# Kernel tuning notes

Measured on AMD Instinct MI355X. Metric: run time of the kernel, lower is better.

## Reference

```python
import math
import jax, jax.numpy as jnp
import numpy as np

B, N, L, D = 4, 16, 1024, 64  # batch, heads, seq len (L1=L2), head dim


def rel_shift(x):
    """Transformer-XL positional shift: [b,n,q,p]->[b,n,q,k] aligning relative positions."""
    b, n, q, k = x.shape
    x = jnp.pad(x, ((0, 0), (0, 0), (0, 0), (1, 0)))  # pad one zero column in front
    x = x.reshape(b, n, k + 1, q)
    return x[:, :, 1:, :].reshape(b, n, q, k)


def setup_inputs() -> dict:
    rng = jax.random.key(0)
    k1, k2, k3, k4, k5 = jax.random.split(rng, 5)
    query_content_biased = jax.random.normal(k1, (B, N, L, D), dtype=jnp.float32)
    query_pos_biased = jax.random.normal(k2, (B, N, L, D), dtype=jnp.float32)
    key = jax.random.normal(k3, (B, N, L, D), dtype=jnp.float32)
    value = jax.random.normal(k4, (B, N, L, D), dtype=jnp.float32)
    pos_encodings = jax.random.normal(k5, (N, L, D), dtype=jnp.float32)
    # causal mask: True = masked (as in torch masked_fill), broadcast over b,n
    mask = jnp.triu(jnp.ones((L, L), dtype=bool), k=1)[None, None]
    return {
        "query_content_biased": query_content_biased,
        "query_pos_biased": query_pos_biased,
        "key": key,
        "value": value,
        "pos_encodings": pos_encodings,
        "mask": mask,
    }


def reference(query_content_biased, query_pos_biased, key, value, pos_encodings, mask):
    # content scores: [b,n,i,j]
    weight = jnp.einsum('bnid,bnjd->bnij', query_content_biased, key)
    # positional scores, shifted into key axis
    pos_scores = jnp.einsum('bnid,npd->bnip', query_pos_biased, pos_encodings)
    weight = weight + rel_shift(pos_scores)
    weight = weight / math.sqrt(key.shape[-1])
    neg = jnp.finfo(weight.dtype).min
    weight = jnp.where(mask, neg, weight)
    weight = jax.nn.softmax(weight, axis=-1)
    weight = jnp.where(mask, jnp.zeros((), weight.dtype), weight)
    # dropout is identity at p=0.0 (eval)
    out = jnp.einsum('bnij,bnjd->bnid', weight, value)
    return (out, weight)
```

## Files before the change

kernel.cpp:

```cpp
#include <hip/hip_runtime.h>
#include <math.h>


#define Bq 4
#define Nh 16
#define Lq 1024
#define Dh 64
#define TQ 16
#define NT 512
#define LROW 1032

#define BAR() asm volatile("s_waitcnt lgkmcnt(0)\n\ts_barrier" ::: "memory")

typedef _Float16 h16;
typedef __attribute__((ext_vector_type(8))) _Float16 f16x8;
typedef __attribute__((ext_vector_type(4))) _Float16 f16x4;
typedef __attribute__((ext_vector_type(4))) float f32x4;

__device__ __forceinline__ f16x8 pack8h(float4 a, float4 b) {
    f16x8 o;
    o[0] = (h16)a.x; o[1] = (h16)a.y; o[2] = (h16)a.z; o[3] = (h16)a.w;
    o[4] = (h16)b.x; o[5] = (h16)b.y; o[6] = (h16)b.z; o[7] = (h16)b.w;
    return o;
}

__device__ __forceinline__ float wave_max(float v) {
    #pragma unroll
    for (int o = 32; o > 0; o >>= 1) v = fmaxf(v, __shfl_xor(v, o));
    return v;
}
__device__ __forceinline__ float wave_sum(float v) {
    #pragma unroll
    for (int o = 32; o > 0; o >>= 1) v += __shfl_xor(v, o);
    return v;
}

__global__ __launch_bounds__(256) void prep_kernel(
    const float* __restrict__ K, const float* __restrict__ P,
    const float* __restrict__ V,
    h16* __restrict__ Kb, h16* __restrict__ Pb, h16* __restrict__ Vt)
{
    __shared__ float t[64][65];
    int b = blockIdx.x;
    if (b < 5120) {
        const float* src; h16* dst; int idx;
        if (b < 4096) { idx = b * 256 + threadIdx.x; src = K; dst = Kb; }
        else          { idx = (b - 4096) * 256 + threadIdx.x; src = P; dst = Pb; }
        float4 v = ((const float4*)src)[idx];
        f16x4 o;
        o[0] = (h16)v.x; o[1] = (h16)v.y; o[2] = (h16)v.z; o[3] = (h16)v.w;
        ((f16x4*)dst)[idx] = o;
        return;
    }
    int bv = b - 5120;
    int bn = bv >> 4, jt = bv & 15;
    int tid = threadIdx.x;
    int d = tid & 63, q = tid >> 6;
    const float* vb = V + ((size_t)(bn * Lq + jt * 64)) * Dh;
    #pragma unroll
    for (int r = 0; r < 16; r++) {
        int jl = r * 4 + q;
        t[jl][d] = vb[(size_t)jl * Dh + d];
    }
    __syncthreads();
    int dd = tid >> 2, jb = (tid & 3) << 4;
    f16x8 s0, s1;
    #pragma unroll
    for (int jj = 0; jj < 8; jj++) {
        s0[jj] = (h16)t[jb + jj][dd];
        s1[jj] = (h16)t[jb + 8 + jj][dd];
    }
    h16* drow = Vt + (((size_t)(bn * 64 + dd)) << 10) + (jt << 6) + jb;
    *(f16x8*)drow = s0;
    *(f16x8*)(drow + 8) = s1;
}

__global__ __launch_bounds__(NT, 8) void relattn_kernel(
    const float* __restrict__ QC, const float* __restrict__ QP,
    const h16* __restrict__ Kb, const h16* __restrict__ Pb,
    const h16* __restrict__ Vtb,
    float* __restrict__ out, float* __restrict__ wout)
{
    __shared__ __align__(16) h16 s_s[TQ][LROW];
    __shared__ __align__(16) float dscr[4][64][4];

    const int tid  = threadIdx.x;
    const int w    = tid >> 6, lane = tid & 63;
    const int ln   = lane & 15, quad = lane >> 4;

    const int bidx = blockIdx.x;
    const int wg   = ((bidx & 7) << 9) | (bidx >> 3);
    const int bn   = wg >> 6, qt = 63 - (wg & 63);
    const int nh   = bn & 15;
    const int i0   = qt << 4, i1 = i0 + 15;

    const float* qcrow = QC + (((size_t)(bn << 10) + i0 + ln) << 6) + (quad << 3);
    const float* qprow = QP + (((size_t)(bn << 10) + i0 + ln) << 6) + (quad << 3);
    f16x8 aC0 = pack8h(*(const float4*)qcrow,        *(const float4*)(qcrow + 4));
    f16x8 aC1 = pack8h(*(const float4*)(qcrow + 32), *(const float4*)(qcrow + 36));
    f16x8 aP0 = pack8h(*(const float4*)qprow,        *(const float4*)(qprow + 4));
    f16x8 aP1 = pack8h(*(const float4*)(qprow + 32), *(const float4*)(qprow + 36));

    {
        f16x8 nf;
        #pragma unroll
        for (int k = 0; k < 8; k++) nf[k] = (h16)-INFINITY;
        int rr0 = tid >> 7;
        int tt  = tid & 127;
        int col = i0 + 16 + (tt << 3);
        if (col < 1024) {
            #pragma unroll
            for (int r = rr0; r < 16; r += 4)
                *(f16x8*)&s_s[r][col] = nf;
        }
    }

    const h16* kbase = Kb + (((size_t)(bn << 10)) << 6) + (quad << 3);
    #pragma unroll
    for (int ct = 0; ct < 8; ct++) {
        int c0 = ((ct << 3) + w) << 4;
        if (c0 <= i1) {
            const h16* kr = kbase + ((size_t)(c0 + ln) << 6);
            f32x4 acc = {0.f, 0.f, 0.f, 0.f};
            acc = __builtin_amdgcn_mfma_f32_16x16x32_f16(aC0, *(const f16x8*)kr,        acc, 0, 0, 0);
            acc = __builtin_amdgcn_mfma_f32_16x16x32_f16(aC1, *(const f16x8*)(kr + 32), acc, 0, 0, 0);
            #pragma unroll
            for (int rg = 0; rg < 4; rg++) {
                int row = (quad << 2) + rg;
                float val = (c0 + ln <= i0 + row) ? acc[rg] : -INFINITY;
                s_s[row][c0 + ln] = (h16)val;
            }
        }
    }
    BAR();

    const h16* pbase = Pb + (((size_t)(nh << 10)) << 6) + (quad << 3);
    #pragma unroll
    for (int ct = 0; ct < 8; ct++) {
        int p0 = ((ct << 3) + w) << 4;
        if (p0 + i0 + 30 >= 1023) {
            const h16* pr = pbase + ((size_t)(p0 + ln) << 6);
            f32x4 acc = {0.f, 0.f, 0.f, 0.f};
            acc = __builtin_amdgcn_mfma_f32_16x16x32_f16(aP0, *(const f16x8*)pr,        acc, 0, 0, 0);
            acc = __builtin_amdgcn_mfma_f32_16x16x32_f16(aP1, *(const f16x8*)(pr + 32), acc, 0, 0, 0);
            int p = p0 + ln;
            #pragma unroll
            for (int rg = 0; rg < 4; rg++) {
                int row = (quad << 2) + rg;
                int j = p + i0 + row - 1023;
                if (j >= 0)
                    s_s[row][j] = (h16)((float)s_s[row][j] + acc[rg]);
            }
        }
    }
    BAR();

    #pragma unroll
    for (int rr = 0; rr < 2; rr++) {
        int r = (w << 1) + rr;
        int i = i0 + r;
        float v[16];
        #pragma unroll
        for (int c = 0; c < 4; c++) {
            f16x4 t = *(f16x4*)&s_s[r][(c << 8) + (lane << 2)];
            v[c * 4 + 0] = (float)t[0]; v[c * 4 + 1] = (float)t[1];
            v[c * 4 + 2] = (float)t[2]; v[c * 4 + 3] = (float)t[3];
        }
        float mx = v[0];
        #pragma unroll
        for (int k = 1; k < 16; k++) mx = fmaxf(mx, v[k]);
        mx = wave_max(mx);
        float sum = 0.f;
        #pragma unroll
        for (int k = 0; k < 16; k++) {
            float t = __expf((v[k] - mx) * 0.125f);
            sum += t;
            v[k] = t;
        }
        sum = wave_sum(sum);
        float inv = __builtin_amdgcn_rcpf(sum);
        float* wrow = wout + (((size_t)(bn << 10) + i) << 10);
        #pragma unroll
        for (int c = 0; c < 4; c++) {
            int j = (c << 8) + (lane << 2);
            f32x4 e;
            e[0] = v[c * 4 + 0] * inv; e[1] = v[c * 4 + 1] * inv;
            e[2] = v[c * 4 + 2] * inv; e[3] = v[c * 4 + 3] * inv;
            __builtin_nontemporal_store(e, (f32x4*)&wrow[j]);
            f16x4 hh;
            hh[0] = (h16)e[0]; hh[1] = (h16)e[1]; hh[2] = (h16)e[2]; hh[3] = (h16)e[3];
            *(f16x4*)&s_s[r][j] = hh;
        }
    }
    BAR();

    f32x4 o = {0.f, 0.f, 0.f, 0.f};
    const int n0 = (w & 3) << 4;
    const int h  = w >> 2;
    const h16* vtb = Vtb + (((size_t)(bn << 6) + n0 + ln) << 10);
    const h16* abase = &s_s[ln][0];
    const int ksteps = (i0 + 16 + 31) >> 5;
    for (int ks = h; ks < ksteps; ks += 2) {
        int k0 = (ks << 5) + (quad << 3);
        f16x8 af = *(const f16x8*)(abase + k0);
        f16x8 vb = *(const f16x8*)(vtb + k0);
        o = __builtin_amdgcn_mfma_f32_16x16x32_f16(af, vb, o, 0, 0, 0);
    }
    if (h == 1)
        *(f32x4*)&dscr[w & 3][lane][0] = o;
    BAR();
    if (h == 0) {
        f32x4 o2 = *(f32x4*)&dscr[w][lane][0];
        o[0] += o2[0]; o[1] += o2[1]; o[2] += o2[2]; o[3] += o2[3];
        float* obase = out + (((size_t)(bn << 10) + i0) << 6);
        #pragma unroll
        for (int rg = 0; rg < 4; rg++)
            __builtin_nontemporal_store(
                o[rg], &obase[((size_t)((quad << 2) + rg) << 6) + n0 + ln]);
    }
}

extern "C" void kernel_launch(void* const* d_in, const int* in_sizes, int n_in,
                              void* d_out, int out_size, void* d_ws, size_t ws_size,
                              hipStream_t stream) {
    const float* qc = (const float*)d_in[0];
    const float* qp = (const float*)d_in[1];
    const float* K  = (const float*)d_in[2];
    const float* V  = (const float*)d_in[3];
    const float* P  = (const float*)d_in[4];

    float* out  = (float*)d_out;
    float* wout = out + (size_t)Bq * Nh * Lq * Dh;

    const size_t NQ = (size_t)Bq * Nh * Lq * Dh;
    const size_t NP = (size_t)Nh * Lq * Dh;
    h16* Kb  = (h16*)d_ws;
    h16* Pb  = Kb + NQ;
    h16* Vtb = Pb + NP;

    prep_kernel<<<4096 + 1024 + 1024, 256, 0, stream>>>(K, P, V, Kb, Pb, Vtb);
    relattn_kernel<<<Bq * Nh * (Lq / TQ), NT, 0, stream>>>(qc, qp, Kb, Pb, Vtb, out, wout);
}
```

Measured before the change: 432.5 us.

## Skip fully masked softmax chunks and zero masked weight tail in prep kernel

The attention kernel now handles only the 256-column chunks of each row up to the causal diagonal chunk, skipping -inf init, softmax and weight stores for fully masked chunks. The zero-filling of the masked upper region of the weight output moves into extra blocks of the prep kernel, which can overlap with the cast/transpose work. This cuts exp, LDS and store work in the main kernel. The same total bytes of weight output are still written, and the prep kernel grows by 4096 blocks.

```diff
diff --git a/kernel.cpp b/kernel.cpp
--- a/kernel.cpp
+++ b/kernel.cpp
@@ -38,23 +38,37 @@
 __global__ __launch_bounds__(256) void prep_kernel(
     const float* __restrict__ K, const float* __restrict__ P,
     const float* __restrict__ V,
-    h16* __restrict__ Kb, h16* __restrict__ Pb, h16* __restrict__ Vt)
+    h16* __restrict__ Kb, h16* __restrict__ Pb, h16* __restrict__ Vt,
+    float* __restrict__ wout)
 {
     __shared__ float t[64][65];
     int b = blockIdx.x;
+    int tid = threadIdx.x;
     if (b < 5120) {
         const float* src; h16* dst; int idx;
-        if (b < 4096) { idx = b * 256 + threadIdx.x; src = K; dst = Kb; }
-        else          { idx = (b - 4096) * 256 + threadIdx.x; src = P; dst = Pb; }
+        if (b < 4096) { idx = b * 256 + tid; src = K; dst = Kb; }
+        else          { idx = (b - 4096) * 256 + tid; src = P; dst = Pb; }
         float4 v = ((const float4*)src)[idx];
         f16x4 o;
         o[0] = (h16)v.x; o[1] = (h16)v.y; o[2] = (h16)v.z; o[3] = (h16)v.w;
         ((f16x4*)dst)[idx] = o;
         return;
     }
+    if (b >= 6144) {
+        int bv = b - 6144;
+        int bn = bv >> 6, qt = bv & 63;
+        int zstart = ((qt >> 4) + 1) << 8;
+        if (zstart >= 1024) return;
+        int row = tid >> 4;
+        int c0  = (tid & 15) << 2;
+        float* wr = wout + (((size_t)(bn << 10) + (qt << 4) + row) << 10);
+        f32x4 z = {0.f, 0.f, 0.f, 0.f};
+        for (int col = zstart + c0; col < 1024; col += 64)
+            __builtin_nontemporal_store(z, (f32x4*)&wr[col]);
+        return;
+    }
     int bv = b - 5120;
     int bn = bv >> 4, jt = bv & 15;
-    int tid = threadIdx.x;
     int d = tid & 63, q = tid >> 6;
     const float* vb = V + ((size_t)(bn * Lq + jt * 64)) * Dh;
     #pragma unroll
@@ -93,6 +107,8 @@
     const int bn   = wg >> 6, qt = 63 - (wg & 63);
     const int nh   = bn & 15;
     const int i0   = qt << 4, i1 = i0 + 15;
+    const int cmax = qt >> 4;
+    const int cend = (cmax + 1) << 8;
 
     const float* qcrow = QC + (((size_t)(bn << 10) + i0 + ln) << 6) + (quad << 3);
     const float* qprow = QP + (((size_t)(bn << 10) + i0 + ln) << 6) + (quad << 3);
@@ -108,7 +124,7 @@
         int rr0 = tid >> 7;
         int tt  = tid & 127;
         int col = i0 + 16 + (tt << 3);
-        if (col < 1024) {
+        if (col < cend) {
             #pragma unroll
             for (int r = rr0; r < 16; r += 4)
                 *(f16x8*)&s_s[r][col] = nf;
@@ -162,34 +178,49 @@
         float v[16];
         #pragma unroll
         for (int c = 0; c < 4; c++) {
-            f16x4 t = *(f16x4*)&s_s[r][(c << 8) + (lane << 2)];
-            v[c * 4 + 0] = (float)t[0]; v[c * 4 + 1] = (float)t[1];
-            v[c * 4 + 2] = (float)t[2]; v[c * 4 + 3] = (float)t[3];
-        }
-        float mx = v[0];
-        #pragma unroll
-        for (int k = 1; k < 16; k++) mx = fmaxf(mx, v[k]);
+            if (c <= cmax) {
+                f16x4 t = *(f16x4*)&s_s[r][(c << 8) + (lane << 2)];
+                v[c * 4 + 0] = (float)t[0]; v[c * 4 + 1] = (float)t[1];
+                v[c * 4 + 2] = (float)t[2]; v[c * 4 + 3] = (float)t[3];
+            }
+        }
+        float mx = -3.0e38f;
+        #pragma unroll
+        for (int c = 0; c < 4; c++) {
+            if (c <= cmax) {
+                #pragma unroll
+                for (int e = 0; e < 4; e++) mx = fmaxf(mx, v[c * 4 + e]);
+            }
+        }
         mx = wave_max(mx);
         float sum = 0.f;
         #pragma unroll
-        for (int k = 0; k < 16; k++) {
-            float t = __expf((v[k] - mx) * 0.125f);
-            sum += t;
-            v[k] = t;
+        for (int c = 0; c < 4; c++) {
+            if (c <= cmax) {
+                #pragma unroll
+                for (int e = 0; e < 4; e++) {
+                    float t = __expf((v[c * 4 + e] - mx) * 0.125f);
+                    sum += t;
+                    v[c * 4 + e] = t;
+                }
+            }
         }
         sum = wave_sum(sum);
         float inv = __builtin_amdgcn_rcpf(sum);
         float* wrow = wout + (((size_t)(bn << 10) + i) << 10);
         #pragma unroll
         for (int c = 0; c < 4; c++) {
-            int j = (c << 8) + (lane << 2);
-            f32x4 e;
-            e[0] = v[c * 4 + 0] * inv; e[1] = v[c * 4 + 1] * inv;
-            e[2] = v[c * 4 + 2] * inv; e[3] = v[c * 4 + 3] * inv;
-            __builtin_nontemporal_store(e, (f32x4*)&wrow[j]);
-            f16x4 hh;
-            hh[0] = (h16)e[0]; hh[1] = (h16)e[1]; hh[2] = (h16)e[2]; hh[3] = (h16)e[3];
-            *(f16x4*)&s_s[r][j] = hh;
+            if (c <= cmax) {
+                int j = (c << 8) + (lane << 2);
+                f32x4 e;
+                e[0] = v[c * 4 + 0] * inv; e[1] = v[c * 4 + 1] * inv;
+                e[2] = v[c * 4 + 2] * inv; e[3] = v[c * 4 + 3] * inv;
+                __builtin_nontemporal_store(e, (f32x4*)&wrow[j]);
+                f16x4 hh;
+                hh[0] = (h16)e[0]; hh[1] = (h16)e[1];
+                hh[2] = (h16)e[2]; hh[3] = (h16)e[3];
+                *(f16x4*)&s_s[r][j] = hh;
+            }
         }
     }
     BAR();
@@ -238,6 +269,6 @@
     h16* Pb  = Kb + NQ;
     h16* Vtb = Pb + NP;
 
-    prep_kernel<<<4096 + 1024 + 1024, 256, 0, stream>>>(K, P, V, Kb, Pb, Vtb);
+    prep_kernel<<<4096 + 1024 + 1024 + 4096, 256, 0, stream>>>(K, P, V, Kb, Pb, Vtb, wout);
     relattn_kernel<<<Bq * Nh * (Lq / TQ), NT, 0, stream>>>(qc, qp, Kb, Pb, Vtb, out, wout);
 }
```

Measured after the change: 440.9 us. Within noise of the previous version (+1.9%).

## Fuse positional scores into content tile via shuffles, prefetch V operands

Applied to the files above, without the earlier changes.

Computes the relative-position scores for each key tile alongside the content scores. It uses two P tiles per 16x16 block and lane shuffles to realise the rel_shift diagonal in registers, instead of a separate pass that read, modified and wrote shared memory. This removes one barrier and the read-modify-write round trip through the f16 score buffer, and it also avoids the rounding from adding in f16. It adds software prefetching of the V and attention operands in the PV loop and lowers the occupancy hint from 8 to 6 to give the extra registers room.

```diff
diff --git a/kernel.cpp b/kernel.cpp
--- a/kernel.cpp
+++ b/kernel.cpp
@@ -42,10 +42,11 @@
 {
     __shared__ float t[64][65];
     int b = blockIdx.x;
+    int tid = threadIdx.x;
     if (b < 5120) {
         const float* src; h16* dst; int idx;
-        if (b < 4096) { idx = b * 256 + threadIdx.x; src = K; dst = Kb; }
-        else          { idx = (b - 4096) * 256 + threadIdx.x; src = P; dst = Pb; }
+        if (b < 4096) { idx = b * 256 + tid; src = K; dst = Kb; }
+        else          { idx = (b - 4096) * 256 + tid; src = P; dst = Pb; }
         float4 v = ((const float4*)src)[idx];
         f16x4 o;
         o[0] = (h16)v.x; o[1] = (h16)v.y; o[2] = (h16)v.z; o[3] = (h16)v.w;
@@ -54,7 +55,6 @@
     }
     int bv = b - 5120;
     int bn = bv >> 4, jt = bv & 15;
-    int tid = threadIdx.x;
     int d = tid & 63, q = tid >> 6;
     const float* vb = V + ((size_t)(bn * Lq + jt * 64)) * Dh;
     #pragma unroll
@@ -75,7 +75,7 @@
     *(f16x8*)(drow + 8) = s1;
 }
 
-__global__ __launch_bounds__(NT, 8) void relattn_kernel(
+__global__ __launch_bounds__(NT, 6) void relattn_kernel(
     const float* __restrict__ QC, const float* __restrict__ QP,
     const h16* __restrict__ Kb, const h16* __restrict__ Pb,
     const h16* __restrict__ Vtb,
@@ -92,7 +92,7 @@
     const int wg   = ((bidx & 7) << 9) | (bidx >> 3);
     const int bn   = wg >> 6, qt = 63 - (wg & 63);
     const int nh   = bn & 15;
-    const int i0   = qt << 4, i1 = i0 + 15;
+    const int i0   = qt << 4;
 
     const float* qcrow = QC + (((size_t)(bn << 10) + i0 + ln) << 6) + (quad << 3);
     const float* qprow = QP + (((size_t)(bn << 10) + i0 + ln) << 6) + (quad << 3);
@@ -116,44 +116,53 @@
     }
 
     const h16* kbase = Kb + (((size_t)(bn << 10)) << 6) + (quad << 3);
+    const h16* pbase = Pb + (((size_t)(nh << 10)) << 6) + (quad << 3);
     #pragma unroll
     for (int ct = 0; ct < 8; ct++) {
         int c0 = ((ct << 3) + w) << 4;
-        if (c0 <= i1) {
+        if (c0 <= i0) {
             const h16* kr = kbase + ((size_t)(c0 + ln) << 6);
-            f32x4 acc = {0.f, 0.f, 0.f, 0.f};
-            acc = __builtin_amdgcn_mfma_f32_16x16x32_f16(aC0, *(const f16x8*)kr,        acc, 0, 0, 0);
-            acc = __builtin_amdgcn_mfma_f32_16x16x32_f16(aC1, *(const f16x8*)(kr + 32), acc, 0, 0, 0);
+            f16x8 k0 = *(const f16x8*)kr, k1 = *(const f16x8*)(kr + 32);
+            int p1 = c0 - i0 + 1008;
+            const h16* pr1 = pbase + ((size_t)(p1 + ln) << 6);
+            f16x8 b10 = *(const f16x8*)pr1, b11 = *(const f16x8*)(pr1 + 32);
+
+            f32x4 accK = {0.f, 0.f, 0.f, 0.f};
+            accK = __builtin_amdgcn_mfma_f32_16x16x32_f16(aC0, k0, accK, 0, 0, 0);
+            accK = __builtin_amdgcn_mfma_f32_16x16x32_f16(aC1, k1, accK, 0, 0, 0);
+
+            f32x4 accT1 = {0.f, 0.f, 0.f, 0.f};
+            accT1 = __builtin_amdgcn_mfma_f32_16x16x32_f16(aP0, b10, accT1, 0, 0, 0);
+            accT1 = __builtin_amdgcn_mfma_f32_16x16x32_f16(aP1, b11, accT1, 0, 0, 0);
+
+            f32x4 accT2 = {0.f, 0.f, 0.f, 0.f};
+            if (c0 < i0) {
+                const h16* pr2 = pr1 + (16ull << 6);
+                f16x8 b20 = *(const f16x8*)pr2, b21 = *(const f16x8*)(pr2 + 32);
+                accT2 = __builtin_amdgcn_mfma_f32_16x16x32_f16(aP0, b20, accT2, 0, 0, 0);
+                accT2 = __builtin_amdgcn_mfma_f32_16x16x32_f16(aP1, b21, accT2, 0, 0, 0);
+            }
+
             #pragma unroll
             for (int rg = 0; rg < 4; rg++) {
                 int row = (quad << 2) + rg;
-                float val = (c0 + ln <= i0 + row) ? acc[rg] : -INFINITY;
-                s_s[row][c0 + ln] = (h16)val;
+                int dl  = (ln + 15 - row) & 15;
+                int src = (lane & 48) | dl;
+                float t1 = __shfl(accT1[rg], src);
+                float t2 = __shfl(accT2[rg], src);
+                float tv = (ln <= row) ? t1 : t2;
+                float val = accK[rg] + tv;
+                s_s[row][c0 + ln] = (h16)((c0 + ln <= i0 + row) ? val : -INFINITY);
             }
         }
     }
     BAR();
 
-    const h16* pbase = Pb + (((size_t)(nh << 10)) << 6) + (quad << 3);
-    #pragma unroll
-    for (int ct = 0; ct < 8; ct++) {
-        int p0 = ((ct << 3) + w) << 4;
-        if (p0 + i0 + 30 >= 1023) {
-            const h16* pr = pbase + ((size_t)(p0 + ln) << 6);
-            f32x4 acc = {0.f, 0.f, 0.f, 0.f};
-            acc = __builtin_amdgcn_mfma_f32_16x16x32_f16(aP0, *(const f16x8*)pr,        acc, 0, 0, 0);
-            acc = __builtin_amdgcn_mfma_f32_16x16x32_f16(aP1, *(const f16x8*)(pr + 32), acc, 0, 0, 0);
-            int p = p0 + ln;
-            #pragma unroll
-            for (int rg = 0; rg < 4; rg++) {
-                int row = (quad << 2) + rg;
-                int j = p + i0 + row - 1023;
-                if (j >= 0)
-                    s_s[row][j] = (h16)((float)s_s[row][j] + acc[rg]);
-            }
-        }
-    }
-    BAR();
+    const int n0 = (w & 3) << 4;
+    const int h  = w >> 2;
+    const h16* vtb = Vtb + (((size_t)(bn << 6) + n0 + ln) << 10);
+    f16x8 vb0 = *(const f16x8*)(vtb + ((h    ) << 5) + (quad << 3));
+    f16x8 vb1 = *(const f16x8*)(vtb + ((h + 2) << 5) + (quad << 3));
 
     #pragma unroll
     for (int rr = 0; rr < 2; rr++) {
@@ -195,16 +204,17 @@
     BAR();
 
     f32x4 o = {0.f, 0.f, 0.f, 0.f};
-    const int n0 = (w & 3) << 4;
-    const int h  = w >> 2;
-    const h16* vtb = Vtb + (((size_t)(bn << 6) + n0 + ln) << 10);
     const h16* abase = &s_s[ln][0];
     const int ksteps = (i0 + 16 + 31) >> 5;
+    f16x8 af = *(const f16x8*)(abase + (h << 5) + (quad << 3));
     for (int ks = h; ks < ksteps; ks += 2) {
-        int k0 = (ks << 5) + (quad << 3);
-        f16x8 af = *(const f16x8*)(abase + k0);
-        f16x8 vb = *(const f16x8*)(vtb + k0);
-        o = __builtin_amdgcn_mfma_f32_16x16x32_f16(af, vb, o, 0, 0, 0);
+        f16x8 afn = {}, vnn = {};
+        if (ks + 2 < ksteps)
+            afn = *(const f16x8*)(abase + ((ks + 2) << 5) + (quad << 3));
+        if (ks + 4 < ksteps)
+            vnn = *(const f16x8*)(vtb + ((ks + 4) << 5) + (quad << 3));
+        o = __builtin_amdgcn_mfma_f32_16x16x32_f16(af, vb0, o, 0, 0, 0);
+        af = afn; vb0 = vb1; vb1 = vnn;
     }
     if (h == 1)
         *(f32x4*)&dscr[w & 3][lane][0] = o;
```

Result: slower. 464.6 us (+7.4%).
